# Optimization experiments

Measured on AMD Instinct MI355X. Metric: run time of the kernel, lower is better.

The kernel has to match this reference:

```python
import jax, jax.numpy as jnp
import numpy as np

ALPHA = 2.0  # snntorch ATan surrogate default alpha
BETA = 0.9
THRESH = 1.0
THRESH_OUT = 20000.0  # decoder i==1 layer per source

@jax.custom_vjp
def atan_spike(u):
    # Heaviside forward, ATan surrogate backward (snntorch default)
    return (u > 0).astype(u.dtype)

def _spike_fwd(u):
    return atan_spike(u), u

def _spike_bwd(u, g):
    grad = (ALPHA / 2.0) / (1.0 + (jnp.pi / 2.0 * ALPHA * u) ** 2)
    return (g * grad,)

atan_spike.defvjp(_spike_fwd, _spike_bwd)

def lif_step(mem, cur, beta, thresh):
    # snntorch Leaky (init_hidden, reset_mechanism='subtract'):
    # reset based on previous mem, then leaky integrate, then fire
    reset = atan_spike(mem - thresh)
    mem = beta * mem + cur - reset * thresh
    spk = atan_spike(mem - thresh)
    return mem, spk

def _linear_init(key, out_f, in_f):
    kw, kb = jax.random.split(key)
    bound = 1.0 / np.sqrt(in_f)
    W = jax.random.uniform(kw, (out_f, in_f), minval=-bound, maxval=bound, dtype=jnp.float32)
    b = jax.random.uniform(kb, (out_f,), minval=-bound, maxval=bound, dtype=jnp.float32)
    return W, b

def setup_inputs() -> dict:
    key = jax.random.key(0)
    ks = jax.random.split(key, 5)
    x = jax.random.normal(ks[0], (8, 128, 512), dtype=jnp.float32)  # [T, B, F]
    W1, b1 = _linear_init(ks[1], 256, 512)  # encoder L1
    W2, b2 = _linear_init(ks[2], 128, 256)  # encoder L2 (output Leaky)
    W3, b3 = _linear_init(ks[3], 256, 128)  # decoder L1
    W4, b4 = _linear_init(ks[4], 512, 256)  # decoder L2 (output Leaky, thresh=20000)
    return dict(x=x, W1=W1, b1=b1, W2=W2, b2=b2, W3=W3, b3=b3, W4=W4, b4=b4)

def reference(x, W1, b1, W2, b2, W3, b3, W4, b4):
    T = x.shape[0]
    # Encoder: whole x is fed every step -> cur1 is constant across steps
    cur1 = x @ W1.T + b1                                   # [T, B, 256]
    m1_0 = jnp.zeros_like(cur1)
    m2_0 = jnp.zeros(cur1.shape[:-1] + (W2.shape[0],), cur1.dtype)

    def enc_step(carry, _):
        m1, m2 = carry
        m1, s1 = lif_step(m1, cur1, BETA, THRESH)
        cur2 = s1 @ W2.T + b2
        m2, s2 = lif_step(m2, cur2, BETA, THRESH)
        return (m1, m2), (s2, m2)

    _, (spk_rec, mem_rec) = jax.lax.scan(enc_step, (m1_0, m2_0), None, length=T)
    # spk_rec: [T, T, B, 128]

    # Decoder: whole spk_rec fed each step -> cur3 constant
    cur3 = spk_rec @ W3.T + b3                             # [T, T, B, 256]
    m3_0 = jnp.zeros_like(cur3)
    m4_0 = jnp.zeros(cur3.shape[:-1] + (W4.shape[0],), cur3.dtype)

    def dec_step(carry, _):
        m3, m4 = carry
        m3, s3 = lif_step(m3, cur3, BETA, THRESH)
        cur4 = s3 @ W4.T + b4
        m4, s4 = lif_step(m4, cur4, BETA, THRESH_OUT)
        return (m3, m4), (s4, m4)

    _, (spk_rec_1, mem_rec_1) = jax.lax.scan(dec_step, (m3_0, m4_0), None, length=T)
    # mem_rec_1, spk_rec_1: [T, T, T, B, 512]
    return mem_rec_1, spk_rec_1
```

## Files before the change

### kernel.cpp

```cpp
#include <hip/hip_runtime.h>
#include <hip/hip_bf16.h>


typedef __attribute__((ext_vector_type(8))) short short8;
typedef __attribute__((ext_vector_type(4))) float f32x4;

__device__ __forceinline__ float bflo(unsigned int u) {
    union { unsigned int u; float f; } v; v.u = u << 16; return v.f;
}
__device__ __forceinline__ float bfhi(unsigned int u) {
    union { unsigned int u; float f; } v; v.u = u & 0xffff0000u; return v.f;
}

__global__ __launch_bounds__(256) void repack_all(
    const float* __restrict__ W1, const float* __restrict__ W2,
    const float* __restrict__ W3, const float* __restrict__ W4,
    float* __restrict__ W1T, float* __restrict__ W2T,
    float* __restrict__ W3T,
    short* __restrict__ BWhi, short* __restrict__ BWlo)
{
    int g = blockIdx.x * 256 + threadIdx.x;
    if (g < 131072) {
        int n = g >> 9, k = g & 511;
        W1T[(((k >> 2) * 256) + n) * 4 + (k & 3)] = W1[g];
    } else if (g < 163840) {
        int i = g - 131072;
        int n = i >> 8, k = i & 255;
        W2T[(((k >> 2) * 128) + n) * 4 + (k & 3)] = W2[i];
    } else if (g < 196608) {
        int i = g - 163840;
        int n = i >> 7, k = i & 127;
        W3T[(((k >> 2) * 256) + n) * 4 + (k & 3)] = W3[i];
    } else if (g < 327680) {
        int i = g - 196608;
        int f = i >> 8, k = i & 255;
        float w = W4[i];
        __hip_bfloat16 hb = __float2bfloat16(w);
        float hf = __bfloat162float(hb);
        __hip_bfloat16 lb = __float2bfloat16(w - hf);
        int kstep = k >> 5, q = (k >> 3) & 3, j = k & 7;
        int dst = (((kstep * 512) + f) * 4 + q) * 8 + j;
        BWhi[dst] = *(short*)&hb;
        BWlo[dst] = *(short*)&lb;
    }
}

__global__ __launch_bounds__(256) void enc1_fused(
    const float* __restrict__ x, const float* __restrict__ W1T,
    const float* __restrict__ b1, __hip_bfloat16* __restrict__ s1)
{
    __shared__ float xs[4][512];
    const int r0 = blockIdx.x * 4, c = threadIdx.x;
    ((float4*)xs)[c]       = ((const float4*)(x + (size_t)r0 * 512))[c];
    ((float4*)xs)[c + 256] = ((const float4*)(x + (size_t)r0 * 512))[c + 256];
    __syncthreads();

    const float4* wv = (const float4*)W1T;
    float acc[4] = {0.f, 0.f, 0.f, 0.f};
    for (int j = 0; j < 128; ++j) {
        float4 w = wv[j * 256 + c];
#pragma unroll
        for (int r = 0; r < 4; ++r) {
            float4 a = ((const float4*)xs[r])[j];
            acc[r] = fmaf(a.x, w.x, acc[r]); acc[r] = fmaf(a.y, w.y, acc[r]);
            acc[r] = fmaf(a.z, w.z, acc[r]); acc[r] = fmaf(a.w, w.w, acc[r]);
        }
    }
    const float b = b1[c];
#pragma unroll
    for (int r = 0; r < 4; ++r) {
        const float cur = __fadd_rn(acc[r], b);
        float m = 0.f;
#pragma unroll
        for (int t = 0; t < 8; ++t) {
            float rst = (__fsub_rn(m, 1.f) > 0.f) ? 1.f : 0.f;
            m = __fsub_rn(__fadd_rn(__fmul_rn(0.9f, m), cur), rst);
            float s = (__fsub_rn(m, 1.f) > 0.f) ? 1.f : 0.f;
            s1[(size_t)t * 262144 + (size_t)(r0 + r) * 256 + c] = __float2bfloat16(s);
        }
    }
}

__global__ __launch_bounds__(256) void enc2_fused(
    const __hip_bfloat16* __restrict__ s1, const float* __restrict__ W2T,
    const float* __restrict__ b2, __hip_bfloat16* __restrict__ spk)
{
    const int i = blockIdx.x * 256 + threadIdx.x;
    const int r = i >> 7, c = i & 127;
    const float4* wv = (const float4*)W2T;
    const uint2* s1v = (const uint2*)s1;

    float acc[8];
#pragma unroll
    for (int t = 0; t < 8; ++t) acc[t] = 0.f;

    for (int j = 0; j < 64; ++j) {
        float4 w = wv[j * 128 + c];
#pragma unroll
        for (int t = 0; t < 8; ++t) {
            uint2 su = s1v[(size_t)t * 65536 + (size_t)r * 64 + j];
            acc[t] = fmaf(bflo(su.x), w.x, acc[t]);
            acc[t] = fmaf(bfhi(su.x), w.y, acc[t]);
            acc[t] = fmaf(bflo(su.y), w.z, acc[t]);
            acc[t] = fmaf(bfhi(su.y), w.w, acc[t]);
        }
    }
    const float bias = b2[c];
    float m = 0.f;
#pragma unroll
    for (int t = 0; t < 8; ++t) {
        float cur = __fadd_rn(acc[t], bias);
        float rst = (__fsub_rn(m, 1.f) > 0.f) ? 1.f : 0.f;
        m = __fsub_rn(__fadd_rn(__fmul_rn(0.9f, m), cur), rst);
        float s = (__fsub_rn(m, 1.f) > 0.f) ? 1.f : 0.f;
        spk[(size_t)t * 131072 + (size_t)r * 128 + c] = __float2bfloat16(s);
    }
}

__global__ __launch_bounds__(256) void dec1_s3(
    const __hip_bfloat16* __restrict__ spk, const float* __restrict__ W3T,
    const float* __restrict__ b3, __hip_bfloat16* __restrict__ s3g)
{
    __shared__ float sp[8][128];
    const int row0 = blockIdx.x * 8, tid = threadIdx.x;
    for (int i = tid; i < 1024; i += 256)
        sp[i >> 7][i & 127] = __bfloat162float(spk[(size_t)row0 * 128 + i]);
    __syncthreads();

    const float4* wv = (const float4*)W3T;
    float acc[8] = {0.f, 0.f, 0.f, 0.f, 0.f, 0.f, 0.f, 0.f};
#pragma unroll
    for (int j = 0; j < 32; ++j) {
        float4 w = wv[j * 256 + tid];
#pragma unroll
        for (int r = 0; r < 8; ++r) {
            float4 a = ((const float4*)sp[r])[j];
            acc[r] = fmaf(a.x, w.x, acc[r]); acc[r] = fmaf(a.y, w.y, acc[r]);
            acc[r] = fmaf(a.z, w.z, acc[r]); acc[r] = fmaf(a.w, w.w, acc[r]);
        }
    }
    const float b = b3[tid];
#pragma unroll
    for (int r = 0; r < 8; ++r) {
        const float cur = __fadd_rn(acc[r], b);
        float m = 0.f;
#pragma unroll
        for (int td = 0; td < 8; ++td) {
            float rst = (__fsub_rn(m, 1.f) > 0.f) ? 1.f : 0.f;
            m = __fsub_rn(__fadd_rn(__fmul_rn(0.9f, m), cur), rst);
            float s = (__fsub_rn(m, 1.f) > 0.f) ? 1.f : 0.f;
            s3g[((size_t)td * 8192 + (row0 + r)) * 256 + tid] = __float2bfloat16(s);
        }
    }
}

__global__ __launch_bounds__(256, 2) void dec2_mfma(
    const __hip_bfloat16* __restrict__ s3g,
    const short* __restrict__ BWhi, const short* __restrict__ BWlo,
    const float* __restrict__ b4,
    float* __restrict__ mem_out, float* __restrict__ spk_out)
{
    const int fb = blockIdx.x & 3, rb = blockIdx.x >> 2;
    const int wv = threadIdx.x >> 6, lane = threadIdx.x & 63;
    const int q = lane >> 4, n = lane & 15;
    const int f0 = fb * 128 + wv * 32;

    const short8* BH = (const short8*)BWhi;
    const short8* BL = (const short8*)BWlo;
    short8 bh0[8], bh1[8], bl0[8], bl1[8];
#pragma unroll
    for (int ks = 0; ks < 8; ++ks) {
        bh0[ks] = BH[(ks * 512 + f0 + 2 * n) * 4 + q];
        bh1[ks] = BH[(ks * 512 + f0 + 2 * n + 1) * 4 + q];
        bl0[ks] = BL[(ks * 512 + f0 + 2 * n) * 4 + q];
        bl1[ks] = BL[(ks * 512 + f0 + 2 * n + 1) * 4 + q];
    }
    const float2 bias = ((const float2*)b4)[(f0 >> 1) + n];
    const short* S = (const short*)s3g;

    for (int rt = 0; rt < 4; ++rt) {
        const int row0 = rb * 64 + rt * 16;
        f32x4 m0 = {0.f, 0.f, 0.f, 0.f}, m1 = {0.f, 0.f, 0.f, 0.f};
#pragma unroll 1
        for (int td = 0; td < 8; ++td) {
            const short* ap = S + ((size_t)(td * 8192 + row0 + n) * 256 + q * 8);
            short8 a[8];
#pragma unroll
            for (int ks = 0; ks < 8; ++ks)
                a[ks] = *(const short8*)(ap + ks * 32);

            f32x4 acc0 = {0.f, 0.f, 0.f, 0.f}, acc1 = {0.f, 0.f, 0.f, 0.f};
#pragma unroll
            for (int ks = 0; ks < 8; ++ks) {
                acc0 = __builtin_amdgcn_mfma_f32_16x16x32_bf16(a[ks], bh0[ks], acc0, 0, 0, 0);
                acc1 = __builtin_amdgcn_mfma_f32_16x16x32_bf16(a[ks], bh1[ks], acc1, 0, 0, 0);
            }
#pragma unroll
            for (int ks = 0; ks < 8; ++ks) {
                acc0 = __builtin_amdgcn_mfma_f32_16x16x32_bf16(a[ks], bl0[ks], acc0, 0, 0, 0);
                acc1 = __builtin_amdgcn_mfma_f32_16x16x32_bf16(a[ks], bl1[ks], acc1, 0, 0, 0);
            }
#pragma unroll
            for (int r = 0; r < 4; ++r) {
                const int row = row0 + q * 4 + r;
                m0[r] = 0.9f * m0[r] + (acc0[r] + bias.x);
                m1[r] = 0.9f * m1[r] + (acc1[r] + bias.y);
                float2 mv; mv.x = m0[r]; mv.y = m1[r];
                ((float2*)(mem_out + ((size_t)td * 8192 + row) * 512))[(f0 >> 1) + n] = mv;
            }
        }
    }

    float4 z; z.x = z.y = z.z = z.w = 0.f;
    float4* sp4 = (float4*)spk_out;
    const int gtid = blockIdx.x * 256 + threadIdx.x;
#pragma unroll
    for (int it = 0; it < 64; ++it)
        sp4[(size_t)it * 131072 + gtid] = z;
}

extern "C" void kernel_launch(void* const* d_in, const int* in_sizes, int n_in,
                              void* d_out, int out_size, void* d_ws, size_t ws_size,
                              hipStream_t stream)
{
    const float* x  = (const float*)d_in[0];
    const float* W1 = (const float*)d_in[1];
    const float* b1 = (const float*)d_in[2];
    const float* W2 = (const float*)d_in[3];
    const float* b2 = (const float*)d_in[4];
    const float* W3 = (const float*)d_in[5];
    const float* b3 = (const float*)d_in[6];
    const float* W4 = (const float*)d_in[7];
    const float* b4 = (const float*)d_in[8];

    char* ws = (char*)d_ws;
    __hip_bfloat16* s1  = (__hip_bfloat16*)(ws);
    __hip_bfloat16* spk = (__hip_bfloat16*)(ws + (4u << 20));
    float* W1T  = (float*)(ws + (6u << 20));
    float* W2T  = (float*)(ws + (6u << 20) + (512u << 10));
    float* W3T  = (float*)(ws + (6u << 20) + (640u << 10));
    short* BWhi = (short*)(ws + (7u << 20) + (256u << 10));
    short* BWlo = (short*)(ws + (7u << 20) + (512u << 10));
    __hip_bfloat16* s3g = (__hip_bfloat16*)(ws + (8u << 20));

    float* mem_out = (float*)d_out;
    float* spk_out = mem_out + 33554432u;

    repack_all<<<1280, 256, 0, stream>>>(W1, W2, W3, W4, W1T, W2T, W3T,
                                         BWhi, BWlo);
    enc1_fused<<<256,  256, 0, stream>>>(x, W1T, b1, s1);
    enc2_fused<<<512,  256, 0, stream>>>(s1, W2T, b2, spk);
    dec1_s3   <<<1024, 256, 0, stream>>>(spk, W3T, b3, s3g);
    dec2_mfma <<<512,  256, 0, stream>>>(s3g, BWhi, BWlo, b4, mem_out, spk_out);
}
```

Measured before the change: 400.3 us.

## Write decoder spikes in MFMA fragment layout and prefetch next timestep A tiles

After: 401.7 us. No clear change (+0.4%).

```diff
diff --git a/kernel.cpp b/kernel.cpp
--- a/kernel.cpp
+++ b/kernel.cpp
@@ -117,52 +117,65 @@
     }
 }
 
-__global__ __launch_bounds__(256) void dec1_s3(
+__global__ __launch_bounds__(256) void dec1_s3A(
     const __hip_bfloat16* __restrict__ spk, const float* __restrict__ W3T,
-    const float* __restrict__ b3, __hip_bfloat16* __restrict__ s3g)
-{
-    __shared__ float sp[8][128];
-    const int row0 = blockIdx.x * 8, tid = threadIdx.x;
-    for (int i = tid; i < 1024; i += 256)
+    const float* __restrict__ b3, unsigned short* __restrict__ s3A)
+{
+    __shared__ float sp[16][128];
+    __shared__ unsigned short tile[16][264];
+    const int rb16 = blockIdx.x, tid = threadIdx.x;
+    const int row0 = rb16 * 16;
+    for (int i = tid; i < 2048; i += 256)
         sp[i >> 7][i & 127] = __bfloat162float(spk[(size_t)row0 * 128 + i]);
     __syncthreads();
 
     const float4* wv = (const float4*)W3T;
-    float acc[8] = {0.f, 0.f, 0.f, 0.f, 0.f, 0.f, 0.f, 0.f};
+    float acc[16];
+#pragma unroll
+    for (int r = 0; r < 16; ++r) acc[r] = 0.f;
 #pragma unroll
     for (int j = 0; j < 32; ++j) {
         float4 w = wv[j * 256 + tid];
 #pragma unroll
-        for (int r = 0; r < 8; ++r) {
+        for (int r = 0; r < 16; ++r) {
             float4 a = ((const float4*)sp[r])[j];
             acc[r] = fmaf(a.x, w.x, acc[r]); acc[r] = fmaf(a.y, w.y, acc[r]);
             acc[r] = fmaf(a.z, w.z, acc[r]); acc[r] = fmaf(a.w, w.w, acc[r]);
         }
     }
     const float b = b3[tid];
-#pragma unroll
-    for (int r = 0; r < 8; ++r) {
-        const float cur = __fadd_rn(acc[r], b);
-        float m = 0.f;
-#pragma unroll
-        for (int td = 0; td < 8; ++td) {
-            float rst = (__fsub_rn(m, 1.f) > 0.f) ? 1.f : 0.f;
-            m = __fsub_rn(__fadd_rn(__fmul_rn(0.9f, m), cur), rst);
-            float s = (__fsub_rn(m, 1.f) > 0.f) ? 1.f : 0.f;
-            s3g[((size_t)td * 8192 + (row0 + r)) * 256 + tid] = __float2bfloat16(s);
-        }
+    float cur[16], m[16];
+#pragma unroll
+    for (int r = 0; r < 16; ++r) { cur[r] = __fadd_rn(acc[r], b); m[r] = 0.f; }
+
+    for (int td = 0; td < 8; ++td) {
+#pragma unroll
+        for (int r = 0; r < 16; ++r) {
+            float rst = (__fsub_rn(m[r], 1.f) > 0.f) ? 1.f : 0.f;
+            m[r] = __fsub_rn(__fadd_rn(__fmul_rn(0.9f, m[r]), cur[r]), rst);
+            tile[r][tid] = (__fsub_rn(m[r], 1.f) > 0.f) ? 0x3F80u : 0u;
+        }
+        __syncthreads();
+#pragma unroll
+        for (int h = 0; h < 2; ++h) {
+            const int F = tid + h * 256;
+            const int ks = F >> 6, q = (F >> 4) & 3, n = F & 15;
+            short8 v = *(const short8*)&tile[n][ks * 32 + q * 8];
+            *(short8*)(s3A + ((((size_t)td * 512 + rb16) * 8 + ks) * 64 + (F & 63)) * 8) = v;
+        }
+        __syncthreads();
     }
 }
 
 __global__ __launch_bounds__(256, 2) void dec2_mfma(
-    const __hip_bfloat16* __restrict__ s3g,
+    const unsigned short* __restrict__ s3A,
     const short* __restrict__ BWhi, const short* __restrict__ BWlo,
     const float* __restrict__ b4,
     float* __restrict__ mem_out, float* __restrict__ spk_out)
 {
     const int fb = blockIdx.x & 3, rb = blockIdx.x >> 2;
     const int wv = threadIdx.x >> 6, lane = threadIdx.x & 63;
-    const int q = lane >> 4, n = lane & 15;
+    const int n = lane & 15;
     const int f0 = fb * 128 + wv * 32;
 
     const short8* BH = (const short8*)BWhi;
@@ -170,24 +183,33 @@
     short8 bh0[8], bh1[8], bl0[8], bl1[8];
 #pragma unroll
     for (int ks = 0; ks < 8; ++ks) {
+        const int q = lane >> 4;
         bh0[ks] = BH[(ks * 512 + f0 + 2 * n) * 4 + q];
         bh1[ks] = BH[(ks * 512 + f0 + 2 * n + 1) * 4 + q];
         bl0[ks] = BL[(ks * 512 + f0 + 2 * n) * 4 + q];
         bl1[ks] = BL[(ks * 512 + f0 + 2 * n + 1) * 4 + q];
     }
     const float2 bias = ((const float2*)b4)[(f0 >> 1) + n];
-    const short* S = (const short*)s3g;
+    const short8* A = (const short8*)s3A;
 
     for (int rt = 0; rt < 4; ++rt) {
-        const int row0 = rb * 64 + rt * 16;
+        const int rt16 = rb * 4 + rt;
+        const size_t abase = (size_t)rt16 * 512 + lane;
         f32x4 m0 = {0.f, 0.f, 0.f, 0.f}, m1 = {0.f, 0.f, 0.f, 0.f};
+
+        short8 a[8], an[8];
+#pragma unroll
+        for (int ks = 0; ks < 8; ++ks)
+            a[ks] = A[abase + ks * 64];
+
 #pragma unroll 1
         for (int td = 0; td < 8; ++td) {
-            const short* ap = S + ((size_t)(td * 8192 + row0 + n) * 256 + q * 8);
-            short8 a[8];
-#pragma unroll
-            for (int ks = 0; ks < 8; ++ks)
-                a[ks] = *(const short8*)(ap + ks * 32);
+            if (td < 7) {
+                const size_t nb = abase + (size_t)(td + 1) * 262144;
+#pragma unroll
+                for (int ks = 0; ks < 8; ++ks)
+                    an[ks] = A[nb + ks * 64];
+            }
 
             f32x4 acc0 = {0.f, 0.f, 0.f, 0.f}, acc1 = {0.f, 0.f, 0.f, 0.f};
 #pragma unroll
@@ -200,14 +222,18 @@
                 acc0 = __builtin_amdgcn_mfma_f32_16x16x32_bf16(a[ks], bl0[ks], acc0, 0, 0, 0);
                 acc1 = __builtin_amdgcn_mfma_f32_16x16x32_bf16(a[ks], bl1[ks], acc1, 0, 0, 0);
             }
+            const int q = lane >> 4;
 #pragma unroll
             for (int r = 0; r < 4; ++r) {
-                const int row = row0 + q * 4 + r;
+                const int row = rt16 * 16 + q * 4 + r;
                 m0[r] = 0.9f * m0[r] + (acc0[r] + bias.x);
                 m1[r] = 0.9f * m1[r] + (acc1[r] + bias.y);
                 float2 mv; mv.x = m0[r]; mv.y = m1[r];
                 ((float2*)(mem_out + ((size_t)td * 8192 + row) * 512))[(f0 >> 1) + n] = mv;
             }
+#pragma unroll
+            for (int ks = 0; ks < 8; ++ks)
+                a[ks] = an[ks];
         }
     }
 
@@ -241,7 +267,7 @@
     float* W3T  = (float*)(ws + (6u << 20) + (640u << 10));
     short* BWhi = (short*)(ws + (7u << 20) + (256u << 10));
     short* BWlo = (short*)(ws + (7u << 20) + (512u << 10));
-    __hip_bfloat16* s3g = (__hip_bfloat16*)(ws + (8u << 20));
+    unsigned short* s3A = (unsigned short*)(ws + (8u << 20));
 
     float* mem_out = (float*)d_out;
     float* spk_out = mem_out + 33554432u;
@@ -250,6 +276,6 @@
                                          BWhi, BWlo);
     enc1_fused<<<256,  256, 0, stream>>>(x, W1T, b1, s1);
     enc2_fused<<<512,  256, 0, stream>>>(s1, W2T, b2, spk);
-    dec1_s3   <<<1024, 256, 0, stream>>>(spk, W3T, b3, s3g);
-    dec2_mfma <<<512,  256, 0, stream>>>(s3g, BWhi, BWlo, b4, mem_out, spk_out);
-}
+    dec1_s3A  <<<512,  256, 0, stream>>>(spk, W3T, b3, s3A);
+    dec2_mfma <<<512,  256, 0, stream>>>(s3A, BWhi, BWlo, b4, mem_out, spk_out);
+}
```
